# Kernel optimization log

Hardware: AMD Instinct MI355X
Metric: run time of the kernel (lower is better)

The kernel has to match this reference:

```python
import jax, jax.numpy as jnp
import numpy as np

B, N, D, H, QV = 8, 1024, 64, 4, 32
C = 2 * D + 1          # combined_dim = 129
K = C // 8             # per-head qk dim = 16
M_PER = 512
M = B * M_PER
NEG = -9e15


def setup_inputs() -> dict:
    key = jax.random.key(0)
    ks = jax.random.split(key, 24)
    s = 0.05
    x = jax.random.normal(ks[0], (B, N, D + 1), jnp.float32)
    h = jax.random.normal(ks[1], (B, N, D), jnp.float32)
    query_vectors = jax.random.normal(ks[2], (M, QV), jnp.float32)
    adj = jax.random.randint(ks[3], (N, N), 0, 2, jnp.int32)
    # unique observed nodes per graph (mimics torch.where on an obs mask)
    perm = jax.vmap(lambda k: jax.random.permutation(k, N))(jax.random.split(ks[4], B))
    nodes_n = perm[:, :M_PER].reshape(-1).astype(jnp.int32)
    nodes_b = jnp.repeat(jnp.arange(B, dtype=jnp.int32), M_PER)
    # per-head attention projections, stacked over heads
    Wq = jax.random.normal(ks[5], (H, C, K), jnp.float32) * s
    bq = jax.random.normal(ks[6], (H, K), jnp.float32) * s
    Wk = jax.random.normal(ks[7], (H, C, K), jnp.float32) * s
    bk = jax.random.normal(ks[8], (H, K), jnp.float32) * s
    Wv = jax.random.normal(ks[9], (H, C, C), jnp.float32) * s
    bv = jax.random.normal(ks[10], (H, C), jnp.float32) * s
    # attentionMLP: Linear(H*C, C) -> ReLU -> Linear(C, C)
    W1 = jax.random.normal(ks[11], (H * C, C), jnp.float32) * s
    b1 = jax.random.normal(ks[12], (C,), jnp.float32) * s
    W2 = jax.random.normal(ks[13], (C, C), jnp.float32) * s
    b2 = jax.random.normal(ks[14], (C,), jnp.float32) * s
    # MLP_Param hypernetwork tensors: W[qvd, in=C, out=D], b[qvd, D]
    Wr = jax.random.normal(ks[15], (QV, C, D), jnp.float32) * s
    br = jax.random.normal(ks[16], (QV, D), jnp.float32) * s
    Wu = jax.random.normal(ks[17], (QV, C, D), jnp.float32) * s
    bu = jax.random.normal(ks[18], (QV, D), jnp.float32) * s
    Wc = jax.random.normal(ks[19], (QV, C, D), jnp.float32) * s
    bc = jax.random.normal(ks[20], (QV, D), jnp.float32) * s
    return dict(x=x, h=h, query_vectors=query_vectors, adj=adj,
                nodes_b=nodes_b, nodes_n=nodes_n,
                Wq=Wq, bq=bq, Wk=Wk, bk=bk, Wv=Wv, bv=bv,
                W1=W1, b1=b1, W2=W2, b2=b2,
                Wr=Wr, br=br, Wu=Wu, bu=bu, Wc=Wc, bc=bc)


def _mlp_param(sel, qv, W, b):
    # hypernetwork: per-node generated linear layer
    Wn = jnp.einsum('md,dio->mio', qv, W)   # [M, C, D]
    bn = qv @ b                              # [M, D]
    return jnp.einsum('mi,mio->mo', sel, Wn) + bn


def reference(x, h, query_vectors, adj, nodes_b, nodes_n,
              Wq, bq, Wk, bk, Wv, bv, W1, b1, W2, b2,
              Wr, br, Wu, bu, Wc, bc):
    combined = jnp.concatenate([x, h], axis=-1)                      # [B,N,C]
    q = jnp.einsum('bnc,hck->hbnk', combined, Wq) + bq[:, None, None, :]
    k = jnp.einsum('bnc,hck->hbnk', combined, Wk) + bk[:, None, None, :]
    v = jnp.einsum('bnc,hcd->hbnd', combined, Wv) + bv[:, None, None, :]
    scores = jnp.einsum('hbnk,hbmk->hbnm', q, k) / jnp.sqrt(jnp.float32(K))
    scores = jax.nn.leaky_relu(scores, 0.2)
    scores = jnp.where(adj == 0, NEG, scores)                        # [N,N] broadcast
    attn = jax.nn.softmax(scores, axis=-1)                           # [H,B,N,N]
    hp = jnp.einsum('hbnm,hbmd->hbnd', attn, v)                      # [H,B,N,C]
    # permute(1,2,0,3).reshape -> concat heads per node
    attn_cat = jnp.transpose(hp, (1, 2, 0, 3)).reshape(B, N, H * C)
    mlp_out = jax.nn.relu(attn_cat @ W1 + b1) @ W2 + b2              # [B,N,C]
    combined = mlp_out + combined                                    # skip connection
    sel = combined[nodes_b, nodes_n]                                 # [M,C]
    r = jax.nn.sigmoid(_mlp_param(sel, query_vectors, Wr, br))       # [M,D]
    u = jax.nn.sigmoid(_mlp_param(sel, query_vectors, Wu, bu))       # [M,D]
    h = h.at[nodes_b, nodes_n].set(r * h[nodes_b, nodes_n])
    combined_new = jnp.concatenate([x, h], axis=-1)
    cand = jnp.tanh(_mlp_param(combined_new[nodes_b, nodes_n], query_vectors, Wc, bc))
    new_h = (1.0 - u) * h[nodes_b, nodes_n] + u * cand               # [M,D]
    return new_h
```

## Files before the change

### kernel.cpp

```cpp
#include <hip/hip_runtime.h>

#define DEVINL __device__ __forceinline__

typedef unsigned short ushort_t;
typedef unsigned long long u64;
typedef __attribute__((ext_vector_type(8))) short short8;
typedef __attribute__((ext_vector_type(8))) unsigned short ushort8;
typedef __attribute__((ext_vector_type(4))) float f32x4;

constexpr int B_ = 8, N_ = 1024, D_ = 64, H_ = 4, QV_ = 32;
constexpr int C_ = 129, K_ = 16, M_ = 4096;
constexpr int CP = 132;
constexpr int NG = B_ * N_;
constexpr int CBS = 160;
constexpr int VTN = 144;
constexpr int KT = 4256;
constexpr int NKT = 133;
constexpr int HPS = 544;

constexpr size_t o_cb    = 0;
constexpr size_t o_qb    = o_cb  + (size_t)NG * CBS / 2;
constexpr size_t o_kb    = o_qb  + (size_t)H_ * NG * 16 / 2;
constexpr size_t o_adjb  = o_kb  + (size_t)H_ * NG * 16 / 2;
constexpr size_t o_wqk   = o_adjb + 32768;
constexpr size_t o_wvt   = o_wqk + (size_t)H_ * 32 * CBS / 2;
constexpr size_t o_vT    = o_wvt + (size_t)H_ * VTN * CBS / 2;
constexpr size_t o_hpb   = o_vT  + (size_t)H_ * VTN * NG / 2;
constexpr size_t o_cpost = o_hpb + (size_t)M_ * HPS / 2;
constexpr size_t o_W1T   = o_cpost + (size_t)M_ * CP;
constexpr size_t o_W2T   = o_W1T + (size_t)144 * HPS / 2;
constexpr size_t o_wtru  = o_W2T + (size_t)144 * 160 / 2;
constexpr size_t o_wtc   = o_wtru + (size_t)128 * KT / 2;
constexpr size_t o_A     = o_wtc + (size_t)64 * KT / 2;
constexpr size_t o_pru   = o_A + (size_t)M_ * KT / 2;
constexpr size_t o_pc2   = o_pru + (size_t)4 * M_ * 128;
constexpr size_t o_cin   = o_vT;

constexpr int SEG0 = NG * CBS;
constexpr int SEG1 = SEG0 + H_ * 32 * CBS;
constexpr int SEG2 = SEG1 + H_ * VTN * CBS;
constexpr int SEG3 = SEG2 + 144 * HPS;
constexpr int SEG4 = SEG3 + 144 * 160;
constexpr int SEG5 = SEG4 + 192 * KT;
constexpr int SEG6 = SEG5 + 1024 * 16 * 64;

DEVINL float4 ld4(const float* p) { return *reinterpret_cast<const float4*>(p); }
DEVINL void st4(float* p, float4 v) { *reinterpret_cast<float4*>(p) = v; }
DEVINL ushort_t f2bf(float f) {
    unsigned int u = __float_as_uint(f);
    u += 0x7FFFu + ((u >> 16) & 1u);
    return (ushort_t)(u >> 16);
}

__global__ void k_prep(const float* __restrict__ x, const float* __restrict__ h,
                       const float* __restrict__ Wq, const float* __restrict__ bq,
                       const float* __restrict__ Wk, const float* __restrict__ bk,
                       const float* __restrict__ Wv, const float* __restrict__ bv,
                       const float* __restrict__ W1, const float* __restrict__ W2,
                       const float* __restrict__ Wr, const float* __restrict__ br,
                       const float* __restrict__ Wu, const float* __restrict__ bu,
                       const float* __restrict__ Wc, const float* __restrict__ bc,
                       const int* __restrict__ adj,
                       ushort_t* __restrict__ cb, ushort_t* __restrict__ wqk,
                       ushort_t* __restrict__ wvt, ushort_t* __restrict__ W1T,
                       ushort_t* __restrict__ W2T, ushort_t* __restrict__ wtru,
                       ushort_t* __restrict__ wtc, u64* __restrict__ ab) {
    int idx = blockIdx.x * 256 + threadIdx.x;
    if (idx < SEG0) {
        int g = idx / CBS, kk = idx - g * CBS;
        float v;
        if (kk < 65) v = x[g * 65 + kk];
        else if (kk < 129) v = h[g * 64 + (kk - 65)];
        else if (kk == 129) v = 1.0f;
        else v = 0.f;
        cb[idx] = f2bf(v);
    } else if (idx < SEG1) {
        int j = idx - SEG0;
        int hh = j / (32 * CBS); int rem = j - hh * 32 * CBS;
        int o = rem / CBS, kk = rem - o * CBS;
        float v = 0.f;
        if (o < 16) {
            if (kk < 129) v = Wq[(size_t)(hh * C_ + kk) * K_ + o];
            else if (kk == 129) v = bq[hh * K_ + o];
        } else {
            int o2 = o - 16;
            if (kk < 129) v = Wk[(size_t)(hh * C_ + kk) * K_ + o2];
            else if (kk == 129) v = bk[hh * K_ + o2];
        }
        wqk[j] = f2bf(v);
    } else if (idx < SEG2) {
        int j = idx - SEG1;
        int hh = j / (VTN * CBS); int rem = j - hh * VTN * CBS;
        int n = rem / CBS, kk = rem - n * CBS;
        float v = 0.f;
        if (n < C_) {
            if (kk < 129) v = Wv[(size_t)(hh * C_ + kk) * C_ + n];
            else if (kk == 129) v = bv[hh * C_ + n];
        }
        wvt[j] = f2bf(v);
    } else if (idx < SEG3) {
        int j = idx - SEG2;
        int o = j / HPS, k = j - o * HPS;
        float v = (o < C_ && k < 516) ? W1[(size_t)k * C_ + o] : 0.f;
        W1T[j] = f2bf(v);
    } else if (idx < SEG4) {
        int j = idx - SEG3;
        int o = j / 160, k = j - o * 160;
        float v = (o < C_ && k < C_) ? W2[(size_t)k * C_ + o] : 0.f;
        W2T[j] = f2bf(v);
    } else if (idx < SEG5) {
        int j = idx - SEG4;
        int row = j / KT, k = j - row * KT;
        float v;
        if (k >= 4224) {
            int d = k - 4224;
            if (row < 64) v = br[d * 64 + row];
            else if (row < 128) v = bu[d * 64 + row - 64];
            else v = bc[d * 64 + row - 128];
        } else {
            int d = k / 132, i = k - d * 132;
            if (i >= 129) v = 0.f;
            else if (row < 64) v = Wr[(size_t)(d * 129 + i) * 64 + row];
            else if (row < 128) v = Wu[(size_t)(d * 129 + i) * 64 + row - 64];
            else v = Wc[(size_t)(d * 129 + i) * 64 + row - 128];
        }
        if (row < 128) wtru[(size_t)row * KT + k] = f2bf(v);
        else wtc[(size_t)(row - 128) * KT + k] = f2bf(v);
    } else if (idx < SEG6) {
        int j = idx - SEG5;
        int word = j >> 6, lane = j & 63;
        int row = word >> 4, wj = word & 15;
        u64 m = __ballot(adj[(size_t)row * N_ + wj * 64 + lane] != 0);
        if (lane == 0) ab[word] = m;
    }
}

__global__ __launch_bounds__(256) void k_qkv(
    const ushort_t* __restrict__ cb, const ushort_t* __restrict__ wqk,
    const ushort_t* __restrict__ wvt,
    ushort_t* __restrict__ qbo, ushort_t* __restrict__ kbo, ushort_t* __restrict__ vTg) {
    const int t = threadIdx.x;
    const int g0 = blockIdx.x * 16;
    const int hh = blockIdx.y;
    const int lane = t & 63, w = t >> 6;
    const int am = lane & 15, aq = lane >> 4;
    short8 cbf[5];
    const ushort_t* Cr = cb + (size_t)(g0 + am) * CBS + aq * 8;
#pragma unroll
    for (int kt = 0; kt < 5; ++kt)
        cbf[kt] = *reinterpret_cast<const short8*>(Cr + kt * 32);
#pragma unroll
    for (int s = 0; s < 3; ++s) {
        int u = w + 4 * s;
        if (u >= 11) break;
        f32x4 acc = f32x4{0.f, 0.f, 0.f, 0.f};
        if (u < 2) {
            const ushort_t* Bp = wqk + ((size_t)(hh * 32 + u * 16 + am)) * CBS + aq * 8;
#pragma unroll
            for (int kt = 0; kt < 5; ++kt)
                acc = __builtin_amdgcn_mfma_f32_16x16x32_bf16(
                    cbf[kt], *reinterpret_cast<const short8*>(Bp + kt * 32), acc, 0, 0, 0);
            ushort_t* dst = u ? kbo : qbo;
#pragma unroll
            for (int i = 0; i < 4; ++i)
                dst[(size_t)(hh * NG + g0 + aq * 4 + i) * 16 + am] = f2bf(acc[i]);
        } else {
            int vt = u - 2;
            const ushort_t* Ap = wvt + ((size_t)(hh * VTN + vt * 16 + am)) * CBS + aq * 8;
#pragma unroll
            for (int kt = 0; kt < 5; ++kt)
                acc = __builtin_amdgcn_mfma_f32_16x16x32_bf16(
                    *reinterpret_cast<const short8*>(Ap + kt * 32), cbf[kt], acc, 0, 0, 0);
#pragma unroll
            for (int i = 0; i < 4; ++i)
                vTg[(size_t)(hh * VTN + vt * 16 + aq * 4 + i) * NG + g0 + am] = f2bf(acc[i]);
        }
    }
}

__global__ __launch_bounds__(256) void k_attn(
    const ushort_t* __restrict__ qb, const ushort_t* __restrict__ kb,
    const ushort_t* __restrict__ vTg, const u64* __restrict__ adjb,
    const int* __restrict__ nodes_b, const int* __restrict__ nodes_n,
    ushort_t* __restrict__ hpb) {
    __shared__ u64 Msk[16][16];
    __shared__ alignas(16) ushort_t Pb[4][16 * 72];
    __shared__ float Ored[3][16 * 144];
    __shared__ float Lpart[4][16];
    __shared__ float Linv[16];
    __shared__ int Nrow[16];
    const int t = threadIdx.x;
    const int bi = blockIdx.x;
    const int mx = ((bi & 7) << 5) + (bi >> 3);
    const int m0 = mx * 16;
    const int hh = blockIdx.y;
    const int b = nodes_b[m0];
    if (t < 16) Nrow[t] = nodes_n[m0 + t];
    __syncthreads();
    { int r = t >> 4, wj = t & 15; Msk[r][wj] = adjb[Nrow[r] * 16 + wj]; }
    const int lane = t & 63, w = t >> 6;
    const int am = lane & 15, aq = lane >> 4;
    short8 qf = short8{0, 0, 0, 0, 0, 0, 0, 0};
    if (aq < 2)
        qf = *reinterpret_cast<const short8*>(&qb[(size_t)(hh * NG + b * N_ + Nrow[am]) * 16 + aq * 8]);
    __syncthreads();
    ushort_t* Pw = Pb[w];
    const ushort_t* kbase = kb + ((size_t)hh * NG + b * N_) * 16;
    f32x4 accv[9];
#pragma unroll
    for (int j = 0; j < 9; ++j) accv[j] = f32x4{0.f, 0.f, 0.f, 0.f};
    float lsum[4] = {0.f, 0.f, 0.f, 0.f};

    for (int ti = 0; ti < 4; ++ti) {
        const int tile = w + 4 * ti;
        const int c0 = tile * 64;
        u64 mrow[4];
#pragma unroll
        for (int i = 0; i < 4; ++i) mrow[i] = Msk[aq * 4 + i][tile];
#pragma unroll
        for (int nt = 0; nt < 4; ++nt) {
            int col = c0 + nt * 16 + am;
            short8 bf = short8{0, 0, 0, 0, 0, 0, 0, 0};
            if (aq < 2)
                bf = *reinterpret_cast<const short8*>(&kbase[(size_t)col * 16 + aq * 8]);
            f32x4 sv = __builtin_amdgcn_mfma_f32_16x16x32_bf16(qf, bf, f32x4{0.f, 0.f, 0.f, 0.f}, 0, 0, 0);
#pragma unroll
            for (int i = 0; i < 4; ++i) {
                float s = sv[i] * 0.25f;
                s = (s >= 0.f) ? s : 0.2f * s;
                float p = ((mrow[i] >> (nt * 16 + am)) & 1ull) ? __expf(s) : 0.f;
                lsum[i] += p;
                Pw[(aq * 4 + i) * 72 + nt * 16 + am] = f2bf(p);
            }
        }
#pragma unroll
        for (int kh = 0; kh < 2; ++kh) {
            short8 af = *reinterpret_cast<const short8*>(&Pw[am * 72 + kh * 32 + aq * 8]);
#pragma unroll
            for (int nt = 0; nt < 9; ++nt) {
                short8 bfr = *reinterpret_cast<const short8*>(
                    &vTg[(size_t)(hh * VTN + nt * 16 + am) * NG + b * N_ + c0 + kh * 32 + aq * 8]);
                accv[nt] = __builtin_amdgcn_mfma_f32_16x16x32_bf16(af, bfr, accv[nt], 0, 0, 0);
            }
        }
    }
#pragma unroll
    for (int i = 0; i < 4; ++i) {
        float v = lsum[i];
        v += __shfl_xor(v, 1); v += __shfl_xor(v, 2);
        v += __shfl_xor(v, 4); v += __shfl_xor(v, 8);
        if (am == 0) Lpart[w][aq * 4 + i] = v;
    }
    if (w > 0) {
#pragma unroll
        for (int nt = 0; nt < 9; ++nt)
#pragma unroll
            for (int i = 0; i < 4; ++i)
                Ored[w - 1][(aq * 4 + i) * 144 + nt * 16 + am] = accv[nt][i];
    }
    __syncthreads();
    if (w == 0) {
        if (t < 16) {
            float s = Lpart[0][t] + Lpart[1][t] + Lpart[2][t] + Lpart[3][t];
            Linv[t] = (s > 0.f) ? 1.f / s : 0.f;
        }
#pragma unroll
        for (int nt = 0; nt < 9; ++nt) {
            int col = nt * 16 + am;
            if (col < C_) {
#pragma unroll
                for (int i = 0; i < 4; ++i) {
                    int row = aq * 4 + i;
                    float val = accv[nt][i] + Ored[0][row * 144 + col]
                              + Ored[1][row * 144 + col] + Ored[2][row * 144 + col];
                    hpb[(size_t)(m0 + row) * HPS + hh * C_ + col] = f2bf(val * Linv[row]);
                }
            }
        }
    }
    if (hh == 3) {
        for (int idx = t; idx < 16 * 28; idx += 256) {
            int rr = idx / 28, cc = 516 + (idx - rr * 28);
            hpb[(size_t)(m0 + rr) * HPS + cc] = 0;
        }
    }
}

__global__ __launch_bounds__(256) void k_mlp(
    const ushort_t* __restrict__ hpb,
    const ushort_t* __restrict__ W1T, const float* __restrict__ b1,
    const ushort_t* __restrict__ W2T, const float* __restrict__ b2,
    const float* __restrict__ x, const float* __restrict__ h,
    const int* __restrict__ nb, const int* __restrict__ nn,
    float* __restrict__ cpost) {
    __shared__ alignas(16) ushort_t Hs[16 * 168];
    const int t = threadIdx.x;
    const int m0 = blockIdx.x * 16;
    const int lane = t & 63, w = t >> 6;
    const int am = lane & 15, aq = lane >> 4;
    f32x4 acc[3];
#pragma unroll
    for (int j = 0; j < 3; ++j) acc[j] = f32x4{0.f, 0.f, 0.f, 0.f};
    const ushort_t* Ar = hpb + (size_t)(m0 + am) * HPS;
    for (int kt = 0; kt < 17; ++kt) {
        short8 af = *reinterpret_cast<const short8*>(Ar + kt * 32 + aq * 8);
#pragma unroll
        for (int j = 0; j < 3; ++j) {
            int nt = w + 4 * j;
            if (nt < 9) {
                short8 bf = *reinterpret_cast<const short8*>(W1T + (size_t)(nt * 16 + am) * HPS + kt * 32 + aq * 8);
                acc[j] = __builtin_amdgcn_mfma_f32_16x16x32_bf16(af, bf, acc[j], 0, 0, 0);
            }
        }
    }
#pragma unroll
    for (int j = 0; j < 3; ++j) {
        int nt = w + 4 * j;
        if (nt < 9) {
            int col = nt * 16 + am;
            float bb = (col < C_) ? b1[col] : 0.f;
#pragma unroll
            for (int i = 0; i < 4; ++i) {
                int row = aq * 4 + i;
                float v = (col < C_) ? fmaxf(acc[j][i] + bb, 0.f) : 0.f;
                Hs[row * 168 + col] = f2bf(v);
            }
        }
    }
    { int row = t >> 4, cc = 144 + (t & 15); Hs[row * 168 + cc] = 0; }
    __syncthreads();
    f32x4 acc2[3];
#pragma unroll
    for (int j = 0; j < 3; ++j) acc2[j] = f32x4{0.f, 0.f, 0.f, 0.f};
    for (int kt = 0; kt < 5; ++kt) {
        short8 af = *reinterpret_cast<const short8*>(&Hs[am * 168 + kt * 32 + aq * 8]);
#pragma unroll
        for (int j = 0; j < 3; ++j) {
            int nt = w + 4 * j;
            if (nt < 9) {
                short8 bf = *reinterpret_cast<const short8*>(W2T + (size_t)(nt * 16 + am) * 160 + kt * 32 + aq * 8);
                acc2[j] = __builtin_amdgcn_mfma_f32_16x16x32_bf16(af, bf, acc2[j], 0, 0, 0);
            }
        }
    }
#pragma unroll
    for (int j = 0; j < 3; ++j) {
        int nt = w + 4 * j;
        if (nt < 9) {
            int col = nt * 16 + am;
            if (col < C_) {
                float bb = b2[col];
#pragma unroll
                for (int i = 0; i < 4; ++i) {
                    int m = m0 + aq * 4 + i;
                    int b = nb[m], n = nn[m];
                    float sk = (col < 65) ? x[(b * N_ + n) * 65 + col]
                                          : h[(b * N_ + n) * D_ + (col - 65)];
                    cpost[(size_t)m * CP + col] = acc2[j][i] + bb + sk;
                }
            }
        }
    }
    if (t < 48) {
        int rr = t / 3, cc = 129 + (t - (t / 3) * 3);
        cpost[(size_t)(m0 + rr) * CP + cc] = 0.f;
    }
}

__global__ __launch_bounds__(256) void k_arow(const float* __restrict__ src,
                                              const float* __restrict__ qv,
                                              ushort_t* __restrict__ A) {
    __shared__ float sq[CP];
    __shared__ float qs[QV_];
    const int t = threadIdx.x;
    const int m = blockIdx.x;
    if (t < CP) sq[t] = src[(size_t)m * CP + t];
    if (t >= 224) qs[t - 224] = qv[m * QV_ + (t - 224)];
    __syncthreads();
    ushort_t* Ar = A + (size_t)m * KT;
    for (int k = t; k < 4224; k += 256) {
        int d = k / 132, i = k - d * 132;
        Ar[k] = f2bf(qs[d] * sq[i]);
    }
    if (t < QV_) Ar[4224 + t] = f2bf(qs[t]);
}

template<int NN>
__global__ __launch_bounds__(256) void k_gemm(const ushort_t* __restrict__ A,
                                              const ushort_t* __restrict__ WT,
                                              float* __restrict__ part) {
    const int t = threadIdx.x;
    const int m0 = blockIdx.x * 16;
    const int z = blockIdx.y;
    const int lane = t & 63, w = t >> 6;
    const int am = lane & 15, aq = lane >> 4;
    constexpr int NTpW = NN / 64;
    const int ktb = z * 34;
    const int kte = (ktb + 34 < NKT) ? ktb + 34 : NKT;
    f32x4 acc[NTpW];
#pragma unroll
    for (int j = 0; j < NTpW; ++j) acc[j] = f32x4{0.f, 0.f, 0.f, 0.f};
    const ushort_t* Ar = A + (size_t)(m0 + am) * KT;
    for (int kt = ktb; kt < kte; ++kt) {
        const int ko = kt * 32 + aq * 8;
        short8 af = *reinterpret_cast<const short8*>(Ar + ko);
#pragma unroll
        for (int j = 0; j < NTpW; ++j) {
            int nt = w + 4 * j;
            short8 bf = *reinterpret_cast<const short8*>(WT + (size_t)(nt * 16 + am) * KT + ko);
            acc[j] = __builtin_amdgcn_mfma_f32_16x16x32_bf16(af, bf, acc[j], 0, 0, 0);
        }
    }
#pragma unroll
    for (int j = 0; j < NTpW; ++j) {
        int n = (w + 4 * j) * 16 + am;
#pragma unroll
        for (int i = 0; i < 4; ++i) {
            int m = m0 + aq * 4 + i;
            part[((size_t)z * M_ + m) * NN + n] = acc[j][i];
        }
    }
}

__global__ void k_build_cin(const float* __restrict__ x, const float* __restrict__ h,
                            const int* __restrict__ nb, const int* __restrict__ nn,
                            const float* __restrict__ pru, float* __restrict__ cin) {
    int idx = blockIdx.x * 256 + threadIdx.x;
    if (idx >= M_ * CP) return;
    int m = idx / CP, i = idx - m * CP;
    int b = nb[m], n = nn[m];
    float val;
    if (i < 65) val = x[(b * N_ + n) * 65 + i];
    else if (i < C_) {
        int o = i - 65;
        const size_t S = (size_t)M_ * 128;
        size_t base = (size_t)m * 128 + o;
        float s = pru[base] + pru[S + base] + pru[2 * S + base] + pru[3 * S + base];
        float rv = 1.f / (1.f + __expf(-s));
        val = rv * h[(b * N_ + n) * D_ + o];
    } else val = 0.f;
    cin[idx] = val;
}

__global__ void k_final(const float* __restrict__ pru, const float* __restrict__ pc,
                        const float* __restrict__ cin, float* __restrict__ out) {
    int idx = blockIdx.x * 256 + threadIdx.x;
    if (idx >= M_ * D_) return;
    int m = idx >> 6, o = idx & 63;
    const size_t Su = (size_t)M_ * 128;
    size_t bu = (size_t)m * 128 + 64 + o;
    float su = pru[bu] + pru[Su + bu] + pru[2 * Su + bu] + pru[3 * Su + bu];
    float uv = 1.f / (1.f + __expf(-su));
    const size_t Sc = (size_t)M_ * 64;
    size_t bc = (size_t)m * 64 + o;
    float sc = pc[bc] + pc[Sc + bc] + pc[2 * Sc + bc] + pc[3 * Sc + bc];
    float cand = tanhf(sc);
    float hn = cin[(size_t)m * CP + 65 + o];
    out[idx] = (1.f - uv) * hn + uv * cand;
}

extern "C" void kernel_launch(void* const* d_in, const int* in_sizes, int n_in,
                              void* d_out, int out_size, void* d_ws, size_t ws_size,
                              hipStream_t stream) {
    const float* x   = (const float*)d_in[0];
    const float* h   = (const float*)d_in[1];
    const float* qv  = (const float*)d_in[2];
    const int*   adj = (const int*)d_in[3];
    const int*   nb  = (const int*)d_in[4];
    const int*   nn  = (const int*)d_in[5];
    const float* Wq  = (const float*)d_in[6];
    const float* bq  = (const float*)d_in[7];
    const float* Wk  = (const float*)d_in[8];
    const float* bk  = (const float*)d_in[9];
    const float* Wv  = (const float*)d_in[10];
    const float* bv  = (const float*)d_in[11];
    const float* W1  = (const float*)d_in[12];
    const float* b1  = (const float*)d_in[13];
    const float* W2  = (const float*)d_in[14];
    const float* b2  = (const float*)d_in[15];
    const float* Wr  = (const float*)d_in[16];
    const float* br  = (const float*)d_in[17];
    const float* Wu  = (const float*)d_in[18];
    const float* bu  = (const float*)d_in[19];
    const float* Wc  = (const float*)d_in[20];
    const float* bc  = (const float*)d_in[21];
    float* ws = (float*)d_ws;
    float* out = (float*)d_out;

    ushort_t* cb   = (ushort_t*)(ws + o_cb);
    ushort_t* qb   = (ushort_t*)(ws + o_qb);
    ushort_t* kb   = (ushort_t*)(ws + o_kb);
    u64*      ab   = (u64*)(ws + o_adjb);
    ushort_t* wqk  = (ushort_t*)(ws + o_wqk);
    ushort_t* wvt  = (ushort_t*)(ws + o_wvt);
    ushort_t* vTg  = (ushort_t*)(ws + o_vT);
    ushort_t* hpb  = (ushort_t*)(ws + o_hpb);
    float* cpost = ws + o_cpost;
    ushort_t* W1T  = (ushort_t*)(ws + o_W1T);
    ushort_t* W2T  = (ushort_t*)(ws + o_W2T);
    ushort_t* wtru = (ushort_t*)(ws + o_wtru);
    ushort_t* wtc  = (ushort_t*)(ws + o_wtc);
    ushort_t* Abuf = (ushort_t*)(ws + o_A);
    float* pru   = ws + o_pru;
    float* pc    = ws + o_pc2;
    float* cin   = ws + o_cin;

    k_prep<<<(SEG6 + 255) / 256, 256, 0, stream>>>(
        x, h, Wq, bq, Wk, bk, Wv, bv, W1, W2, Wr, br, Wu, bu, Wc, bc, adj,
        cb, wqk, wvt, W1T, W2T, wtru, wtc, ab);
    k_qkv<<<dim3(NG / 16, H_), 256, 0, stream>>>(cb, wqk, wvt, qb, kb, vTg);
    k_attn<<<dim3(M_ / 16, H_), 256, 0, stream>>>(qb, kb, vTg, ab, nb, nn, hpb);
    k_mlp<<<M_ / 16, 256, 0, stream>>>(hpb, W1T, b1, W2T, b2, x, h, nb, nn, cpost);
    k_arow<<<M_, 256, 0, stream>>>(cpost, qv, Abuf);
    k_gemm<128><<<dim3(M_ / 16, 4), 256, 0, stream>>>(Abuf, wtru, pru);
    k_build_cin<<<(M_ * CP + 255) / 256, 256, 0, stream>>>(x, h, nb, nn, pru, cin);
    k_arow<<<M_, 256, 0, stream>>>(cin, qv, Abuf);
    k_gemm<64><<<dim3(M_ / 16, 4), 256, 0, stream>>>(Abuf, wtc, pc);
    k_final<<<(M_ * D_ + 255) / 256, 256, 0, stream>>>(pru, pc, cin, out);
}
```

Before: 290.2 us.

## Tile A and weight buffers by k-chunk and give each GEMM block 32 rows

The A matrix and the hypernetwork weight matrices are stored k-tile-major: 32-element chunks, with all rows of a k-tile contiguous. Each wave's loads therefore touch one contiguous region instead of rows strided by KT. The GEMM block now covers 32 rows instead of 16, so each weight fragment feeds two MFMAs and weight traffic is halved. This doubles the accumulator registers and halves the grid size, which may reduce occupancy.

```diff
diff --git a/kernel.cpp b/kernel.cpp
--- a/kernel.cpp
+++ b/kernel.cpp
@@ -124,8 +124,9 @@
             else if (row < 128) v = Wu[(size_t)(d * 129 + i) * 64 + row - 64];
             else v = Wc[(size_t)(d * 129 + i) * 64 + row - 128];
         }
-        if (row < 128) wtru[(size_t)row * KT + k] = f2bf(v);
-        else wtc[(size_t)(row - 128) * KT + k] = f2bf(v);
+        int kt = k >> 5, kj = k & 31;
+        if (row < 128) wtru[((size_t)kt * 128 + row) * 32 + kj] = f2bf(v);
+        else wtc[((size_t)kt * 64 + (row - 128)) * 32 + kj] = f2bf(v);
     } else if (idx < SEG6) {
         int j = idx - SEG5;
         int word = j >> 6, lane = j & 63;
@@ -377,12 +378,11 @@
     if (t < CP) sq[t] = src[(size_t)m * CP + t];
     if (t >= 224) qs[t - 224] = qv[m * QV_ + (t - 224)];
     __syncthreads();
-    ushort_t* Ar = A + (size_t)m * KT;
     for (int k = t; k < 4224; k += 256) {
         int d = k / 132, i = k - d * 132;
-        Ar[k] = f2bf(qs[d] * sq[i]);
-    }
-    if (t < QV_) Ar[4224 + t] = f2bf(qs[t]);
+        A[((size_t)(k >> 5) * M_ + m) * 32 + (k & 31)] = f2bf(qs[d] * sq[i]);
+    }
+    if (t < QV_) A[((size_t)132 * M_ + m) * 32 + t] = f2bf(qs[t]);
 }
 
 template<int NN>
@@ -390,35 +390,41 @@
                                               const ushort_t* __restrict__ WT,
                                               float* __restrict__ part) {
     const int t = threadIdx.x;
-    const int m0 = blockIdx.x * 16;
+    const int m0 = blockIdx.x * 32;
     const int z = blockIdx.y;
     const int lane = t & 63, w = t >> 6;
     const int am = lane & 15, aq = lane >> 4;
     constexpr int NTpW = NN / 64;
     const int ktb = z * 34;
     const int kte = (ktb + 34 < NKT) ? ktb + 34 : NKT;
-    f32x4 acc[NTpW];
-#pragma unroll
-    for (int j = 0; j < NTpW; ++j) acc[j] = f32x4{0.f, 0.f, 0.f, 0.f};
-    const ushort_t* Ar = A + (size_t)(m0 + am) * KT;
+    f32x4 acc[2][NTpW];
+#pragma unroll
+    for (int r2 = 0; r2 < 2; ++r2)
+#pragma unroll
+        for (int j = 0; j < NTpW; ++j) acc[r2][j] = f32x4{0.f, 0.f, 0.f, 0.f};
     for (int kt = ktb; kt < kte; ++kt) {
-        const int ko = kt * 32 + aq * 8;
-        short8 af = *reinterpret_cast<const short8*>(Ar + ko);
+        const ushort_t* Ab = A + ((size_t)kt * M_ + m0) * 32 + aq * 8;
+        short8 a0 = *reinterpret_cast<const short8*>(Ab + am * 32);
+        short8 a1 = *reinterpret_cast<const short8*>(Ab + (am + 16) * 32);
+        const ushort_t* Bb = WT + (size_t)kt * NN * 32 + am * 32 + aq * 8;
 #pragma unroll
         for (int j = 0; j < NTpW; ++j) {
             int nt = w + 4 * j;
-            short8 bf = *reinterpret_cast<const short8*>(WT + (size_t)(nt * 16 + am) * KT + ko);
-            acc[j] = __builtin_amdgcn_mfma_f32_16x16x32_bf16(af, bf, acc[j], 0, 0, 0);
+            short8 bf = *reinterpret_cast<const short8*>(Bb + nt * 16 * 32);
+            acc[0][j] = __builtin_amdgcn_mfma_f32_16x16x32_bf16(a0, bf, acc[0][j], 0, 0, 0);
+            acc[1][j] = __builtin_amdgcn_mfma_f32_16x16x32_bf16(a1, bf, acc[1][j], 0, 0, 0);
         }
     }
 #pragma unroll
     for (int j = 0; j < NTpW; ++j) {
         int n = (w + 4 * j) * 16 + am;
 #pragma unroll
-        for (int i = 0; i < 4; ++i) {
-            int m = m0 + aq * 4 + i;
-            part[((size_t)z * M_ + m) * NN + n] = acc[j][i];
-        }
+        for (int r2 = 0; r2 < 2; ++r2)
+#pragma unroll
+            for (int i = 0; i < 4; ++i) {
+                int m = m0 + r2 * 16 + aq * 4 + i;
+                part[((size_t)z * M_ + m) * NN + n] = acc[r2][j][i];
+            }
     }
 }
 
@@ -512,9 +518,9 @@
     k_attn<<<dim3(M_ / 16, H_), 256, 0, stream>>>(qb, kb, vTg, ab, nb, nn, hpb);
     k_mlp<<<M_ / 16, 256, 0, stream>>>(hpb, W1T, b1, W2T, b2, x, h, nb, nn, cpost);
     k_arow<<<M_, 256, 0, stream>>>(cpost, qv, Abuf);
-    k_gemm<128><<<dim3(M_ / 16, 4), 256, 0, stream>>>(Abuf, wtru, pru);
+    k_gemm<128><<<dim3(M_ / 32, 4), 256, 0, stream>>>(Abuf, wtru, pru);
     k_build_cin<<<(M_ * CP + 255) / 256, 256, 0, stream>>>(x, h, nb, nn, pru, cin);
     k_arow<<<M_, 256, 0, stream>>>(cin, qv, Abuf);
-    k_gemm<64><<<dim3(M_ / 16, 4), 256, 0, stream>>>(Abuf, wtc, pc);
+    k_gemm<64><<<dim3(M_ / 32, 4), 256, 0, stream>>>(Abuf, wtc, pc);
     k_final<<<(M_ * D_ + 255) / 256, 256, 0, stream>>>(pru, pc, cin, out);
 }
```

After: 266.4 us. -8.2%, faster.
